# Optimization experiments

Hardware: AMD Instinct MI355X
Metric: run time of the kernel (lower is better)

## Reference

```python
import jax, jax.numpy as jnp
import numpy as np

N_ENT, N_REL, DIM, N_BASES = 100000, 474, 200, 100
N_EDGES, N_TRIPLES = 500000, 200000


def setup_inputs() -> dict:
    key = jax.random.key(0)
    ks = jax.random.split(key, 12)
    s = np.sqrt(2.0 / (1 + 0.01 ** 2))  # kaiming-ish scale (exact init irrelevant for correctness baseline)
    return {
        "entity_embeds": jax.random.normal(ks[0], (N_ENT, DIM), jnp.float32) * 0.05,
        "bases": jax.random.normal(ks[1], (N_BASES, DIM), jnp.float32) * 0.05,
        "coefficients": jax.random.normal(ks[2], (N_REL, N_BASES), jnp.float32) * 0.05,
        "w1": jax.random.normal(ks[3], (3, DIM, DIM), jnp.float32) * (s / np.sqrt(DIM)),
        "rw1": jax.random.normal(ks[4], (DIM, DIM), jnp.float32) * (s / np.sqrt(DIM)),
        "w2": jax.random.normal(ks[5], (3, DIM, DIM), jnp.float32) * (s / np.sqrt(DIM)),
        "rw2": jax.random.normal(ks[6], (DIM, DIM), jnp.float32) * (s / np.sqrt(DIM)),
        "ent_ids": jnp.arange(N_ENT, dtype=jnp.int32),
        "edge_index": jax.random.randint(ks[7], (2, N_EDGES), 0, N_ENT, jnp.int32),
        "edge_type": jax.random.randint(ks[8], (N_EDGES,), 0, N_REL, jnp.int32),
        "y": jax.random.randint(ks[9], (N_EDGES,), 0, 3, jnp.int32),
        "triples": jax.random.randint(ks[10], (N_TRIPLES, 3), 0, N_REL, jnp.int32),
    }


def _compgcn_layer(x, r, W, RW, edge_index, edge_type, y, n_nodes):
    # message: x_j + r[edge_type], then per-edge-direction linear transform W[y]
    msgs = x[edge_index[0]] + r[edge_type]            # [E, d]
    t = jnp.einsum('ed,kdf->kef', msgs, W)            # [3, E, d] (avoids [E,d,d] gather)
    sel = jnp.where(y[:, None] == 0, t[0], jnp.where(y[:, None] == 1, t[1], t[2]))  # [E, d]
    agg = jax.ops.segment_sum(sel, edge_index[1], num_segments=n_nodes)  # aggr='add'
    return jnp.tanh(agg), r @ RW


def reference(entity_embeds, bases, coefficients, w1, rw1, w2, rw2,
              ent_ids, edge_index, edge_type, y, triples):
    # encode (eval mode: dropout is identity)
    x = entity_embeds[ent_ids]
    r = coefficients @ bases                          # [num_relations, d]
    n_nodes = x.shape[0]
    x, r = _compgcn_layer(x, r, w1, rw1, edge_index, edge_type, y, n_nodes)
    x, r = _compgcn_layer(x, r, w2, rw2, edge_index, edge_type, y, n_nodes)
    # L2 normalize (torch eps=1e-12)
    x = x / jnp.maximum(jnp.linalg.norm(x, axis=1, keepdims=True), 1e-12)
    # decode: TransE-style L1 distance, sigmoid
    h = x[triples[:, 0]]
    rel = r[triples[:, 1]]
    t = x[triples[:, 2]]
    scores = jnp.sum(jnp.abs(h + rel - t), axis=1)    # norm p=1
    return jax.nn.sigmoid(scores)
```

## Files before the change

kernel.cpp:

```cpp
#include <hip/hip_runtime.h>
#include <math.h>


#define NENT     100000
#define NREL     474
#define DIM      200
#define NBASES   100
#define NEDGES   500000
#define NTRIPLES 200000

#define CHUNK    50000
#define NCHUNKS  2
#define SD       608
#define KD       608
#define NTILES   13

#define OFF_R1    0UL
#define OFF_R2    379904UL
#define OFF_R3    759808UL
#define OFF_DEG   1139712UL
#define OFF_CUR   1540096UL
#define OFF_CSR   1940480UL
#define OFF_BSUM  2340864UL
#define OFF_BOFF  2341888UL
#define OFF_CSRC  2342912UL
#define OFF_CRY   4343808UL
#define OFF_WT1   6344704UL
#define OFF_WT2   6598656UL
#define OFF_ENTB  6852608UL
#define OFF_X1B   46853120UL
#define OFF_SBUF  86853632UL
#define OFF_X2    147654144UL

typedef __attribute__((ext_vector_type(8))) short bf16x8;
typedef __attribute__((ext_vector_type(4))) float f32x4;

__device__ inline unsigned short f2bf(float f) {
    unsigned u = __float_as_uint(f);
    return (unsigned short)((u + 0x7FFFu + ((u >> 16) & 1u)) >> 16);
}
__device__ inline float bf2f(unsigned short s) {
    return __uint_as_float(((unsigned)s) << 16);
}

__global__ __launch_bounds__(256) void k_small_gemm(
    const float* __restrict__ A, const float* __restrict__ B,
    float* __restrict__ C, int M, int K, int N)
{
    int tid = blockIdx.x * blockDim.x + threadIdx.x;
    if (tid >= M * N) return;
    int row = tid / N, col = tid - row * N;
    const float* a = A + (long)row * K;
    float acc = 0.f;
    int k = 0;
    for (; k + 4 <= K; k += 4) {
        acc = fmaf(a[k + 0], B[(k + 0) * N + col], acc);
        acc = fmaf(a[k + 1], B[(k + 1) * N + col], acc);
        acc = fmaf(a[k + 2], B[(k + 2) * N + col], acc);
        acc = fmaf(a[k + 3], B[(k + 3) * N + col], acc);
    }
    for (; k < K; ++k) acc = fmaf(a[k], B[k * N + col], acc);
    C[tid] = acc;
}

__global__ __launch_bounds__(256) void k_wt(const float* __restrict__ W,
                                            unsigned short* __restrict__ Wt)
{
    int i = blockIdx.x * 256 + threadIdx.x;
    if (i >= 208 * 608) return;
    int c = i / 608, k = i - c * 608;
    float v = (c < 200 && k < 600) ? W[k * 200 + c] : 0.f;
    Wt[i] = f2bf(v);
}

__global__ __launch_bounds__(256) void k_entb(const float4* __restrict__ ent,
                                              const int* __restrict__ ids,
                                              ushort4* __restrict__ out)
{
    int i = blockIdx.x * 256 + threadIdx.x;
    if (i >= NENT * 50) return;
    int node = i / 50, j = i - node * 50;
    float4 v = ent[(long)ids[node] * 50 + j];
    ushort4 o;
    o.x = f2bf(v.x); o.y = f2bf(v.y); o.z = f2bf(v.z); o.w = f2bf(v.w);
    out[i] = o;
}

__global__ __launch_bounds__(256) void k_hist(const int* __restrict__ ei, int* __restrict__ deg)
{
    int e = blockIdx.x * blockDim.x + threadIdx.x;
    if (e >= NEDGES) return;
    atomicAdd(&deg[ei[NEDGES + e]], 1);
}

__global__ __launch_bounds__(256) void k_scanA(
    const int* __restrict__ deg, int* __restrict__ out, int* __restrict__ bsum)
{
    __shared__ int sd[256];
    int t = threadIdx.x, b = blockIdx.x;
    int base = b * 1024 + t * 4;
    int v0 = (base + 0 < NENT) ? deg[base + 0] : 0;
    int v1 = (base + 1 < NENT) ? deg[base + 1] : 0;
    int v2 = (base + 2 < NENT) ? deg[base + 2] : 0;
    int v3 = (base + 3 < NENT) ? deg[base + 3] : 0;
    int s = v0 + v1 + v2 + v3;
    sd[t] = s; __syncthreads();
    for (int off = 1; off < 256; off <<= 1) {
        int x = (t >= off) ? sd[t - off] : 0;
        __syncthreads();
        sd[t] += x;
        __syncthreads();
    }
    int excl = sd[t] - s;
    if (base + 0 < NENT) out[base + 0] = excl;
    if (base + 1 < NENT) out[base + 1] = excl + v0;
    if (base + 2 < NENT) out[base + 2] = excl + v0 + v1;
    if (base + 3 < NENT) out[base + 3] = excl + v0 + v1 + v2;
    if (t == 255) bsum[b] = sd[255];
}

__global__ __launch_bounds__(128) void k_scanB(
    const int* __restrict__ bsum, int* __restrict__ boff, int nb)
{
    __shared__ int sd[128];
    int t = threadIdx.x;
    int s = (t < nb) ? bsum[t] : 0;
    sd[t] = s; __syncthreads();
    for (int off = 1; off < 128; off <<= 1) {
        int x = (t >= off) ? sd[t - off] : 0;
        __syncthreads();
        sd[t] += x;
        __syncthreads();
    }
    if (t < nb) boff[t] = sd[t] - s;
}

__global__ __launch_bounds__(256) void k_scanC(int* __restrict__ csr, const int* __restrict__ boff)
{
    int t = threadIdx.x, b = blockIdx.x;
    int base = b * 1024 + t * 4;
    int add = boff[b];
    #pragma unroll
    for (int i = 0; i < 4; ++i)
        if (base + i < NENT) csr[base + i] += add;
    if (b == 0 && t == 0) csr[NENT] = NEDGES;
}

__global__ __launch_bounds__(256) void k_scatter(
    const int* __restrict__ ei, const int* __restrict__ et, const int* __restrict__ y,
    const int* __restrict__ csr, int* __restrict__ cur,
    int* __restrict__ csrc, int* __restrict__ cry)
{
    int e = blockIdx.x * blockDim.x + threadIdx.x;
    if (e >= NEDGES) return;
    int dst = ei[NEDGES + e];
    int pos = csr[dst] + atomicAdd(&cur[dst], 1);
    csrc[pos] = ei[e];
    cry[pos]  = et[e] | (y[e] << 16);
}

__global__ __launch_bounds__(256) void k_accum(
    const unsigned short* __restrict__ xb,
    const float4* __restrict__ r,
    const int* __restrict__ csr, const int* __restrict__ csrc, const int* __restrict__ cry,
    unsigned short* __restrict__ S, int nodeBase)
{
    int wv   = (blockIdx.x * blockDim.x + threadIdx.x) >> 6;
    int lane = threadIdx.x & 63;
    unsigned short* srow = S + (long)wv * SD;
    if (lane >= 50) {
        if (lane == 50) {
            uint4 z; z.x = z.y = z.z = z.w = 0u;
            *(uint4*)(srow + 600) = z;
        }
        return;
    }
    int v = nodeBase + wv;
    int start = csr[v], end = csr[v + 1];
    float4 a0 = {0,0,0,0}, a1 = {0,0,0,0}, a2 = {0,0,0,0};
    for (int e = start; e < end; ++e) {
        int src = csrc[e];
        int ry  = cry[e];
        int rel = ry & 0xFFFF;
        int k   = ry >> 16;
        ushort4 xv = *(const ushort4*)(xb + (long)src * 200 + lane * 4);
        float4  rv = r[(long)rel * 50 + lane];
        float mx = bf2f(xv.x) + rv.x, my = bf2f(xv.y) + rv.y;
        float mz = bf2f(xv.z) + rv.z, mw = bf2f(xv.w) + rv.w;
        if (k == 0)      { a0.x += mx; a0.y += my; a0.z += mz; a0.w += mw; }
        else if (k == 1) { a1.x += mx; a1.y += my; a1.z += mz; a1.w += mw; }
        else             { a2.x += mx; a2.y += my; a2.z += mz; a2.w += mw; }
    }
    ushort4 o;
    o.x = f2bf(a0.x); o.y = f2bf(a0.y); o.z = f2bf(a0.z); o.w = f2bf(a0.w);
    *(ushort4*)(srow +   0 + lane * 4) = o;
    o.x = f2bf(a1.x); o.y = f2bf(a1.y); o.z = f2bf(a1.z); o.w = f2bf(a1.w);
    *(ushort4*)(srow + 200 + lane * 4) = o;
    o.x = f2bf(a2.x); o.y = f2bf(a2.y); o.z = f2bf(a2.z); o.w = f2bf(a2.w);
    *(ushort4*)(srow + 400 + lane * 4) = o;
}

template<int OUTBF>
__global__ __launch_bounds__(256) void k_gemm_mfma(
    const unsigned short* __restrict__ S, const unsigned short* __restrict__ Wt,
    void* __restrict__ Xout, int nrows, int rowBase)
{
    int wid  = threadIdx.x >> 6;
    int lane = threadIdx.x & 63;
    int l15  = lane & 15;
    int l4   = lane >> 4;
    int row0 = (blockIdx.x * 4 + wid) * 32;
    int ra = row0 + l15;       if (ra >= nrows) ra = nrows - 1;
    int rb = row0 + 16 + l15;  if (rb >= nrows) rb = nrows - 1;
    const unsigned short* pa = S  + (long)ra * SD + l4 * 8;
    const unsigned short* pb = S  + (long)rb * SD + l4 * 8;
    const unsigned short* pw = Wt + (long)l15 * KD + l4 * 8;

    f32x4 acc0[NTILES] = {};
    f32x4 acc1[NTILES] = {};
    for (int kt = 0; kt < 19; ++kt) {
        bf16x8 a0 = *(const bf16x8*)(pa + kt * 32);
        bf16x8 a1 = *(const bf16x8*)(pb + kt * 32);
        #pragma unroll
        for (int nt = 0; nt < NTILES; ++nt) {
            bf16x8 b = *(const bf16x8*)(pw + nt * 16 * KD + kt * 32);
            acc0[nt] = __builtin_amdgcn_mfma_f32_16x16x32_bf16(a0, b, acc0[nt], 0, 0, 0);
            acc1[nt] = __builtin_amdgcn_mfma_f32_16x16x32_bf16(a1, b, acc1[nt], 0, 0, 0);
        }
    }
    #pragma unroll
    for (int nt = 0; nt < NTILES; ++nt) {
        int col = nt * 16 + l15;
        bool cok = (col < DIM);
        #pragma unroll
        for (int i = 0; i < 4; ++i) {
            int r0 = row0 + l4 * 4 + i;
            if (cok && r0 < nrows) {
                float v = tanhf(acc0[nt][i]);
                if (OUTBF) ((unsigned short*)Xout)[(long)(rowBase + r0) * DIM + col] = f2bf(v);
                else       ((float*)Xout)[(long)(rowBase + r0) * DIM + col] = v;
            }
            int r1 = r0 + 16;
            if (cok && r1 < nrows) {
                float v = tanhf(acc1[nt][i]);
                if (OUTBF) ((unsigned short*)Xout)[(long)(rowBase + r1) * DIM + col] = f2bf(v);
                else       ((float*)Xout)[(long)(rowBase + r1) * DIM + col] = v;
            }
        }
    }
}

__global__ __launch_bounds__(256) void k_norm(float4* __restrict__ x)
{
    int wv   = (blockIdx.x * blockDim.x + threadIdx.x) >> 6;
    int lane = threadIdx.x & 63;
    float4 v = {0,0,0,0};
    if (lane < 50) v = x[(long)wv * 50 + lane];
    float ss = v.x*v.x + v.y*v.y + v.z*v.z + v.w*v.w;
    for (int off = 1; off < 64; off <<= 1) ss += __shfl_xor(ss, off);
    float scale = 1.f / fmaxf(sqrtf(ss), 1e-12f);
    if (lane < 50) {
        v.x *= scale; v.y *= scale; v.z *= scale; v.w *= scale;
        x[(long)wv * 50 + lane] = v;
    }
}

__global__ __launch_bounds__(256) void k_score(
    const float4* __restrict__ x, const float4* __restrict__ r,
    const int* __restrict__ tri, float* __restrict__ out)
{
    int wv   = (blockIdx.x * blockDim.x + threadIdx.x) >> 6;
    int lane = threadIdx.x & 63;
    if (wv >= NTRIPLES) return;
    int h = tri[wv * 3 + 0], rel = tri[wv * 3 + 1], t = tri[wv * 3 + 2];
    float p = 0.f;
    if (lane < 50) {
        float4 hv = x[(long)h * 50 + lane];
        float4 rv = r[(long)rel * 50 + lane];
        float4 tv = x[(long)t * 50 + lane];
        p = fabsf(hv.x + rv.x - tv.x) + fabsf(hv.y + rv.y - tv.y)
          + fabsf(hv.z + rv.z - tv.z) + fabsf(hv.w + rv.w - tv.w);
    }
    for (int off = 1; off < 64; off <<= 1) p += __shfl_xor(p, off);
    if (lane == 0) out[wv] = 1.f / (1.f + expf(-p));
}

extern "C" void kernel_launch(void* const* d_in, const int* in_sizes, int n_in,
                              void* d_out, int out_size, void* d_ws, size_t ws_size,
                              hipStream_t stream)
{
    const float* ent    = (const float*)d_in[0];
    const float* bases  = (const float*)d_in[1];
    const float* coeff  = (const float*)d_in[2];
    const float* w1     = (const float*)d_in[3];
    const float* rw1    = (const float*)d_in[4];
    const float* w2     = (const float*)d_in[5];
    const float* rw2    = (const float*)d_in[6];
    const int*   entids = (const int*)d_in[7];
    const int*   ei     = (const int*)d_in[8];
    const int*   etype  = (const int*)d_in[9];
    const int*   yv     = (const int*)d_in[10];
    const int*   tri    = (const int*)d_in[11];
    float* out = (float*)d_out;

    char* ws = (char*)d_ws;
    float* r1   = (float*)(ws + OFF_R1);
    float* r2   = (float*)(ws + OFF_R2);
    float* r3   = (float*)(ws + OFF_R3);
    int* deg    = (int*)(ws + OFF_DEG);
    int* cur    = (int*)(ws + OFF_CUR);
    int* csr    = (int*)(ws + OFF_CSR);
    int* bsum   = (int*)(ws + OFF_BSUM);
    int* boff   = (int*)(ws + OFF_BOFF);
    int* csrc   = (int*)(ws + OFF_CSRC);
    int* cry    = (int*)(ws + OFF_CRY);
    unsigned short* wt1  = (unsigned short*)(ws + OFF_WT1);
    unsigned short* wt2  = (unsigned short*)(ws + OFF_WT2);
    unsigned short* entb = (unsigned short*)(ws + OFF_ENTB);
    unsigned short* x1b  = (unsigned short*)(ws + OFF_X1B);
    unsigned short* Sbuf = (unsigned short*)(ws + OFF_SBUF);
    float* x2   = (float*)(ws + OFF_X2);

    hipMemsetAsync(ws + OFF_DEG, 0, OFF_CSR - OFF_DEG, stream);

    {
        int tot = NREL * DIM;
        int nb = (tot + 255) / 256;
        k_small_gemm<<<nb, 256, 0, stream>>>(coeff, bases, r1, NREL, NBASES, DIM);
        k_small_gemm<<<nb, 256, 0, stream>>>(r1, rw1, r2, NREL, DIM, DIM);
        k_small_gemm<<<nb, 256, 0, stream>>>(r2, rw2, r3, NREL, DIM, DIM);
    }

    k_wt<<<(208 * 608 + 255) / 256, 256, 0, stream>>>(w1, wt1);
    k_wt<<<(208 * 608 + 255) / 256, 256, 0, stream>>>(w2, wt2);
    k_entb<<<(NENT * 50 + 255) / 256, 256, 0, stream>>>(
        (const float4*)ent, entids, (ushort4*)entb);

    k_hist<<<(NEDGES + 255) / 256, 256, 0, stream>>>(ei, deg);
    int nScanBlocks = (NENT + 1023) / 1024;
    k_scanA<<<nScanBlocks, 256, 0, stream>>>(deg, csr, bsum);
    k_scanB<<<1, 128, 0, stream>>>(bsum, boff, nScanBlocks);
    k_scanC<<<nScanBlocks, 256, 0, stream>>>(csr, boff);
    k_scatter<<<(NEDGES + 255) / 256, 256, 0, stream>>>(ei, etype, yv, csr, cur, csrc, cry);

    int gblocks = (CHUNK + 127) / 128;

    for (int c = 0; c < NCHUNKS; ++c) {
        int base = c * CHUNK;
        k_accum<<<CHUNK * 64 / 256, 256, 0, stream>>>(entb, (const float4*)r1,
                                                      csr, csrc, cry, Sbuf, base);
        k_gemm_mfma<1><<<gblocks, 256, 0, stream>>>(Sbuf, wt1, (void*)x1b, CHUNK, base);
    }
    for (int c = 0; c < NCHUNKS; ++c) {
        int base = c * CHUNK;
        k_accum<<<CHUNK * 64 / 256, 256, 0, stream>>>(x1b, (const float4*)r2,
                                                      csr, csrc, cry, Sbuf, base);
        k_gemm_mfma<0><<<gblocks, 256, 0, stream>>>(Sbuf, wt2, (void*)x2, CHUNK, base);
    }

    k_norm<<<NENT / 4, 256, 0, stream>>>((float4*)x2);
    k_score<<<(NTRIPLES + 3) / 4, 256, 0, stream>>>(
        (const float4*)x2, (const float4*)r3, tri, out);
}
```

Baseline: 846.1 us.

## Split GEMM columns across waves and read relation embeddings as bf16

The MFMA GEMM is retiled so each block covers 32 rows, with four waves each owning 16 rows by 7 column tiles instead of 32 rows by all 13 tiles. This cuts accumulator registers per wave, raising occupancy and launching 4x more blocks, at the cost of reloading A rows across column-split waves. Separately, relation embeddings are converted to bf16 once, which halves gather bytes for r in the accumulate kernel but slightly reduces precision. The weight padding grows to 224 columns to fit two 7-tile halves.

```diff
diff --git a/kernel.cpp b/kernel.cpp
--- a/kernel.cpp
+++ b/kernel.cpp
@@ -13,24 +13,27 @@
 #define NCHUNKS  2
 #define SD       608
 #define KD       608
-#define NTILES   13
+#define NPAD     224
+#define NTILW    7
 
 #define OFF_R1    0UL
-#define OFF_R2    379904UL
-#define OFF_R3    759808UL
-#define OFF_DEG   1139712UL
-#define OFF_CUR   1540096UL
-#define OFF_CSR   1940480UL
-#define OFF_BSUM  2340864UL
-#define OFF_BOFF  2341888UL
-#define OFF_CSRC  2342912UL
-#define OFF_CRY   4343808UL
-#define OFF_WT1   6344704UL
-#define OFF_WT2   6598656UL
-#define OFF_ENTB  6852608UL
-#define OFF_X1B   46853120UL
-#define OFF_SBUF  86853632UL
-#define OFF_X2    147654144UL
+#define OFF_R2    380928UL
+#define OFF_R3    761856UL
+#define OFF_R1B   1142784UL
+#define OFF_R2B   1335296UL
+#define OFF_DEG   1527808UL
+#define OFF_CUR   1929216UL
+#define OFF_CSR   2330624UL
+#define OFF_BSUM  2732032UL
+#define OFF_BOFF  2736128UL
+#define OFF_CSRC  2740224UL
+#define OFF_CRY   4743168UL
+#define OFF_WT1   6746112UL
+#define OFF_WT2   7020544UL
+#define OFF_ENTB  7294976UL
+#define OFF_X1B   47296512UL
+#define OFF_SBUF  87298048UL
+#define OFF_X2    148099072UL
 
 typedef __attribute__((ext_vector_type(8))) short bf16x8;
 typedef __attribute__((ext_vector_type(4))) float f32x4;
@@ -63,12 +66,19 @@
     C[tid] = acc;
 }
 
+__global__ __launch_bounds__(256) void k_rb(const float* __restrict__ in,
+                                            unsigned short* __restrict__ out, int n)
+{
+    int i = blockIdx.x * 256 + threadIdx.x;
+    if (i < n) out[i] = f2bf(in[i]);
+}
+
 __global__ __launch_bounds__(256) void k_wt(const float* __restrict__ W,
                                             unsigned short* __restrict__ Wt)
 {
     int i = blockIdx.x * 256 + threadIdx.x;
-    if (i >= 208 * 608) return;
-    int c = i / 608, k = i - c * 608;
+    if (i >= NPAD * KD) return;
+    int c = i / KD, k = i - c * KD;
     float v = (c < 200 && k < 600) ? W[k * 200 + c] : 0.f;
     Wt[i] = f2bf(v);
 }
@@ -161,7 +171,7 @@
 
 __global__ __launch_bounds__(256) void k_accum(
     const unsigned short* __restrict__ xb,
-    const float4* __restrict__ r,
+    const unsigned short* __restrict__ rb,
     const int* __restrict__ csr, const int* __restrict__ csrc, const int* __restrict__ cry,
     unsigned short* __restrict__ S, int nodeBase)
 {
@@ -184,9 +194,9 @@
         int rel = ry & 0xFFFF;
         int k   = ry >> 16;
         ushort4 xv = *(const ushort4*)(xb + (long)src * 200 + lane * 4);
-        float4  rv = r[(long)rel * 50 + lane];
-        float mx = bf2f(xv.x) + rv.x, my = bf2f(xv.y) + rv.y;
-        float mz = bf2f(xv.z) + rv.z, mw = bf2f(xv.w) + rv.w;
+        ushort4 rv = *(const ushort4*)(rb + (long)rel * 200 + lane * 4);
+        float mx = bf2f(xv.x) + bf2f(rv.x), my = bf2f(xv.y) + bf2f(rv.y);
+        float mz = bf2f(xv.z) + bf2f(rv.z), mw = bf2f(xv.w) + bf2f(rv.w);
         if (k == 0)      { a0.x += mx; a0.y += my; a0.z += mz; a0.w += mw; }
         else if (k == 1) { a1.x += mx; a1.y += my; a1.z += mz; a1.w += mw; }
         else             { a2.x += mx; a2.y += my; a2.z += mz; a2.w += mw; }
@@ -209,42 +219,32 @@
     int lane = threadIdx.x & 63;
     int l15  = lane & 15;
     int l4   = lane >> 4;
-    int row0 = (blockIdx.x * 4 + wid) * 32;
-    int ra = row0 + l15;       if (ra >= nrows) ra = nrows - 1;
-    int rb = row0 + 16 + l15;  if (rb >= nrows) rb = nrows - 1;
+    int row0 = blockIdx.x * 32 + (wid & 1) * 16;
+    int nt0  = (wid >> 1) * NTILW;
+    int ra = row0 + l15; if (ra >= nrows) ra = nrows - 1;
     const unsigned short* pa = S  + (long)ra * SD + l4 * 8;
-    const unsigned short* pb = S  + (long)rb * SD + l4 * 8;
-    const unsigned short* pw = Wt + (long)l15 * KD + l4 * 8;
-
-    f32x4 acc0[NTILES] = {};
-    f32x4 acc1[NTILES] = {};
+    const unsigned short* pw = Wt + (long)(nt0 * 16 + l15) * KD + l4 * 8;
+
+    f32x4 acc[NTILW] = {};
     for (int kt = 0; kt < 19; ++kt) {
-        bf16x8 a0 = *(const bf16x8*)(pa + kt * 32);
-        bf16x8 a1 = *(const bf16x8*)(pb + kt * 32);
+        bf16x8 a = *(const bf16x8*)(pa + kt * 32);
         #pragma unroll
-        for (int nt = 0; nt < NTILES; ++nt) {
+        for (int nt = 0; nt < NTILW; ++nt) {
             bf16x8 b = *(const bf16x8*)(pw + nt * 16 * KD + kt * 32);
-            acc0[nt] = __builtin_amdgcn_mfma_f32_16x16x32_bf16(a0, b, acc0[nt], 0, 0, 0);
-            acc1[nt] = __builtin_amdgcn_mfma_f32_16x16x32_bf16(a1, b, acc1[nt], 0, 0, 0);
+            acc[nt] = __builtin_amdgcn_mfma_f32_16x16x32_bf16(a, b, acc[nt], 0, 0, 0);
         }
     }
     #pragma unroll
-    for (int nt = 0; nt < NTILES; ++nt) {
-        int col = nt * 16 + l15;
+    for (int nt = 0; nt < NTILW; ++nt) {
+        int col = (nt0 + nt) * 16 + l15;
         bool cok = (col < DIM);
         #pragma unroll
         for (int i = 0; i < 4; ++i) {
-            int r0 = row0 + l4 * 4 + i;
-            if (cok && r0 < nrows) {
-                float v = tanhf(acc0[nt][i]);
-                if (OUTBF) ((unsigned short*)Xout)[(long)(rowBase + r0) * DIM + col] = f2bf(v);
-                else       ((float*)Xout)[(long)(rowBase + r0) * DIM + col] = v;
-            }
-            int r1 = r0 + 16;
-            if (cok && r1 < nrows) {
-                float v = tanhf(acc1[nt][i]);
-                if (OUTBF) ((unsigned short*)Xout)[(long)(rowBase + r1) * DIM + col] = f2bf(v);
-                else       ((float*)Xout)[(long)(rowBase + r1) * DIM + col] = v;
+            int r = row0 + l4 * 4 + i;
+            if (cok && r < nrows) {
+                float v = tanhf(acc[nt][i]);
+                if (OUTBF) ((unsigned short*)Xout)[(long)(rowBase + r) * DIM + col] = f2bf(v);
+                else       ((float*)Xout)[(long)(rowBase + r) * DIM + col] = v;
             }
         }
     }
@@ -307,6 +307,8 @@
     float* r1   = (float*)(ws + OFF_R1);
     float* r2   = (float*)(ws + OFF_R2);
     float* r3   = (float*)(ws + OFF_R3);
+    unsigned short* r1b = (unsigned short*)(ws + OFF_R1B);
+    unsigned short* r2b = (unsigned short*)(ws + OFF_R2B);
     int* deg    = (int*)(ws + OFF_DEG);
     int* cur    = (int*)(ws + OFF_CUR);
     int* csr    = (int*)(ws + OFF_CSR);
@@ -329,10 +331,12 @@
         k_small_gemm<<<nb, 256, 0, stream>>>(coeff, bases, r1, NREL, NBASES, DIM);
         k_small_gemm<<<nb, 256, 0, stream>>>(r1, rw1, r2, NREL, DIM, DIM);
         k_small_gemm<<<nb, 256, 0, stream>>>(r2, rw2, r3, NREL, DIM, DIM);
-    }
-
-    k_wt<<<(208 * 608 + 255) / 256, 256, 0, stream>>>(w1, wt1);
-    k_wt<<<(208 * 608 + 255) / 256, 256, 0, stream>>>(w2, wt2);
+        k_rb<<<nb, 256, 0, stream>>>(r1, r1b, tot);
+        k_rb<<<nb, 256, 0, stream>>>(r2, r2b, tot);
+    }
+
+    k_wt<<<(NPAD * KD + 255) / 256, 256, 0, stream>>>(w1, wt1);
+    k_wt<<<(NPAD * KD + 255) / 256, 256, 0, stream>>>(w2, wt2);
     k_entb<<<(NENT * 50 + 255) / 256, 256, 0, stream>>>(
         (const float4*)ent, entids, (ushort4*)entb);
 
@@ -343,17 +347,17 @@
     k_scanC<<<nScanBlocks, 256, 0, stream>>>(csr, boff);
     k_scatter<<<(NEDGES + 255) / 256, 256, 0, stream>>>(ei, etype, yv, csr, cur, csrc, cry);
 
-    int gblocks = (CHUNK + 127) / 128;
+    int gblocks = (CHUNK + 31) / 32;
 
     for (int c = 0; c < NCHUNKS; ++c) {
         int base = c * CHUNK;
-        k_accum<<<CHUNK * 64 / 256, 256, 0, stream>>>(entb, (const float4*)r1,
+        k_accum<<<CHUNK * 64 / 256, 256, 0, stream>>>(entb, r1b,
                                                       csr, csrc, cry, Sbuf, base);
         k_gemm_mfma<1><<<gblocks, 256, 0, stream>>>(Sbuf, wt1, (void*)x1b, CHUNK, base);
     }
     for (int c = 0; c < NCHUNKS; ++c) {
         int base = c * CHUNK;
-        k_accum<<<CHUNK * 64 / 256, 256, 0, stream>>>(x1b, (const float4*)r2,
+        k_accum<<<CHUNK * 64 / 256, 256, 0, stream>>>(x1b, r2b,
                                                       csr, csrc, cry, Sbuf, base);
         k_gemm_mfma<0><<<gblocks, 256, 0, stream>>>(Sbuf, wt2, (void*)x2, CHUNK, base);
     }
```

New measurement: 799.0 us. -5.6%, faster.
